# Performance work log

Measured on AMD Instinct MI355X. Metric: run time of the kernel, lower is better.

Reference implementation:

```python
import jax, jax.numpy as jnp
import numpy as np

N_ADDR, N_TX = 150000, 200000
IN_DIM, HID, HEADS = 64, 32, 4
DIM = HID // HEADS
E_AT, E_TA, E_AA = 1000000, 1000000, 500000
SLOPE = 0.2  # HANConv default negative_slope


def setup_inputs() -> dict:
    key = jax.random.key(0)
    ks = jax.random.split(key, 16)
    f = lambda k, shape, s: jax.random.normal(k, shape, dtype=jnp.float32) * s
    return {
        "x_addr": f(ks[0], (N_ADDR, IN_DIM), 1.0),
        "x_tx": f(ks[1], (N_TX, IN_DIM), 1.0),
        "e_at_src": jax.random.randint(ks[2], (E_AT,), 0, N_ADDR, dtype=jnp.int32),
        "e_at_dst": jax.random.randint(ks[3], (E_AT,), 0, N_TX, dtype=jnp.int32),
        "e_ta_src": jax.random.randint(ks[4], (E_TA,), 0, N_TX, dtype=jnp.int32),
        "e_ta_dst": jax.random.randint(ks[5], (E_TA,), 0, N_ADDR, dtype=jnp.int32),
        "e_aa_src": jax.random.randint(ks[6], (E_AA,), 0, N_ADDR, dtype=jnp.int32),
        "e_aa_dst": jax.random.randint(ks[7], (E_AA,), 0, N_ADDR, dtype=jnp.int32),
        "pW1": f(ks[8], (2, IN_DIM, HID), 0.1),      # layer-1 proj per node type [addr, tx]
        "pb1": jnp.zeros((2, HID), jnp.float32),
        "pW23": f(ks[9], (2, 2, HID, HID), 0.1),     # [layer-1, node_type]
        "pb23": jnp.zeros((2, 2, HID), jnp.float32),
        "att_src": f(ks[10], (3, 3, HEADS, DIM), 0.1),  # [layer, edge_type, H, D]
        "att_dst": f(ks[11], (3, 3, HEADS, DIM), 0.1),
        "kW": f(ks[12], (3, HID, HID), 0.1),         # semantic k_lin per layer
        "kb": jnp.zeros((3, HID), jnp.float32),
        "q": f(ks[13], (3, HID), 0.1),               # semantic query per layer
        "linW": f(ks[14], (HID, 2), 0.1),
        "linb": jnp.zeros((2,), jnp.float32),
    }


def _edge_softmax(logits, dst, n):
    # numerically stable segment softmax over destination neighborhoods
    m = jax.ops.segment_max(logits, dst, num_segments=n)          # [n, H]
    m = jnp.where(jnp.isfinite(m), m, 0.0)
    e = jnp.exp(logits - m[dst])
    s = jax.ops.segment_sum(e, dst, num_segments=n)
    return e / (s[dst] + 1e-16)


def _relation(h_src, h_dst, src, dst, a_s, a_d, n_dst):
    alpha_src = jnp.einsum('nhd,hd->nh', h_src, a_s)
    alpha_dst = jnp.einsum('nhd,hd->nh', h_dst, a_d)
    logit = alpha_src[src] + alpha_dst[dst]                        # [E, H]
    logit = jnp.where(logit >= 0, logit, SLOPE * logit)            # leaky_relu
    alpha = _edge_softmax(logit, dst, n_dst)
    msg = h_src[src] * alpha[:, :, None]                           # [E, H, D]
    out = jax.ops.segment_sum(msg, dst, num_segments=n_dst)        # [n_dst, H, D]
    return jax.nn.relu(out.reshape(n_dst, HID))


def _semantic(xs, kW, kb, q):
    # xs: [R, N, F]; semantic-level attention over R relations (PyG `group`)
    t = jnp.tanh(xs @ kW + kb).mean(axis=1)       # [R, F]
    attn = jax.nn.softmax((t * q).sum(-1))        # [R]
    return jnp.einsum('r,rnf->nf', attn, xs)


def _han_layer(x_a, x_t, Wa, ba, Wt, bt, a_s, a_d, kW, kb, q, edges):
    h_a = (x_a @ Wa + ba).reshape(-1, HEADS, DIM)
    h_t = (x_t @ Wt + bt).reshape(-1, HEADS, DIM)
    o_tx = _relation(h_a, h_t, edges[0], edges[1], a_s[0], a_d[0], N_TX)
    o_a1 = _relation(h_t, h_a, edges[2], edges[3], a_s[1], a_d[1], N_ADDR)
    o_a2 = _relation(h_a, h_a, edges[4], edges[5], a_s[2], a_d[2], N_ADDR)
    new_a = _semantic(jnp.stack([o_a1, o_a2]), kW, kb, q)
    new_t = _semantic(o_tx[None], kW, kb, q)
    return new_a, new_t


def reference(x_addr, x_tx, e_at_src, e_at_dst, e_ta_src, e_ta_dst,
              e_aa_src, e_aa_dst, pW1, pb1, pW23, pb23, att_src, att_dst,
              kW, kb, q, linW, linb):
    edges = (e_at_src, e_at_dst, e_ta_src, e_ta_dst, e_aa_src, e_aa_dst)
    a, t = _han_layer(x_addr, x_tx, pW1[0], pb1[0], pW1[1], pb1[1],
                      att_src[0], att_dst[0], kW[0], kb[0], q[0], edges)
    a, t = jax.nn.relu(a), jax.nn.relu(t)  # wrapper relu; dropout = eval identity
    for l in range(2):
        a, t = _han_layer(a, t, pW23[l, 0], pb23[l, 0], pW23[l, 1], pb23[l, 1],
                          att_src[l + 1], att_dst[l + 1],
                          kW[l + 1], kb[l + 1], q[l + 1], edges)
        a, t = jax.nn.relu(a), jax.nn.relu(t)
    return a @ linW + linb
```

## Files before the change

### kernel.cpp

```cpp
#include <hip/hip_runtime.h>
#include <hip/hip_bf16.h>
#include <hip/hip_fp16.h>

#define NA 150000
#define NT 200000
#define E_AT 1000000
#define E_TA 1000000
#define E_AA 500000

#define CHK 4096
#define CAP 8192
#define P_AT 391
#define P_TA 293
#define P_AA 293
#define NBINS (P_AT + P_TA + P_AA)
#define CB_AT 245
#define CB_TA 245
#define CB_AA 123
#define NBBIN (CB_AT + CB_TA + CB_AA)

#define GB_AT 6250
#define GB_TA 4688
#define GB_AA 4688

#define GA32 4688
#define GT32 6250
#define NB_SEM 586

#define WO_W1   0
#define WO_B1   4096
#define WO_W23  4160
#define WO_B23  8256
#define WO_AS   8384
#define WO_AD   8672
#define WO_KW   8960
#define WO_KB   12032
#define WO_Q    12128
#define WO_LW   12224
#define WO_LB   12288

__device__ __forceinline__ float ldf(const void* p, long i, int f32) {
    if (f32) return ((const float*)p)[i];
    unsigned int u = ((const unsigned short*)p)[i];
    union { unsigned int ui; float f; } v; v.ui = u << 16;
    return v.f;
}
__device__ __forceinline__ float bf2f(unsigned short u) {
    union { unsigned int ui; float f; } v; v.ui = ((unsigned int)u) << 16;
    return v.f;
}
__device__ __forceinline__ float h2f(unsigned short u) {
    return __half2float(__ushort_as_half(u));
}
__device__ __forceinline__ unsigned short f2h(float x) {
    return __half_as_ushort(__float2half(x));
}
__device__ __forceinline__ float ftanh(float x) {
    x = fminf(fmaxf(x, -9.f), 9.f);
    float e = __expf(2.f * x);
    return (e - 1.f) / (e + 1.f);
}

__global__ void k_init(const void* __restrict__ x,
                       const void* __restrict__ pW1, const void* __restrict__ pb1,
                       const void* __restrict__ pW23, const void* __restrict__ pb23,
                       const void* __restrict__ attS, const void* __restrict__ attD,
                       const void* __restrict__ kW, const void* __restrict__ kb,
                       const void* __restrict__ qv, const void* __restrict__ linW,
                       const void* __restrict__ linb,
                       float* __restrict__ wts, int* __restrict__ flagp,
                       int* __restrict__ gcnt, float* __restrict__ sem) {
    __shared__ int cnt;
    const int t = threadIdx.x;
    if (t == 0) cnt = 0;
    __syncthreads();
    const unsigned short* u = (const unsigned short*)x;
    int wild = 0;
    for (int i = t; i < 4096; i += 256) {
        unsigned short v = u[i];
        int e = (v >> 7) & 0xFF;
        if (e > 133 || (e != 0 && e < 100)) wild++;
        else if (e == 0 && (v & 0x7F)) wild++;
    }
    atomicAdd(&cnt, wild);
    __syncthreads();
    const int f32 = (cnt > 1024) ? 1 : 0;
    if (t == 0) *flagp = f32;
    if (t < 8) sem[t] = 0.f;
    for (int i = t; i < 1024; i += 256) gcnt[i] = 0;
    for (int i = t; i < 4096; i += 256) wts[WO_W1 + i]  = ldf(pW1, i, f32);
    for (int i = t; i < 64;   i += 256) wts[WO_B1 + i]  = ldf(pb1, i, f32);
    for (int i = t; i < 4096; i += 256) wts[WO_W23 + i] = ldf(pW23, i, f32);
    for (int i = t; i < 128;  i += 256) wts[WO_B23 + i] = ldf(pb23, i, f32);
    for (int i = t; i < 288;  i += 256) wts[WO_AS + i]  = ldf(attS, i, f32);
    for (int i = t; i < 288;  i += 256) wts[WO_AD + i]  = ldf(attD, i, f32);
    for (int i = t; i < 3072; i += 256) wts[WO_KW + i]  = ldf(kW, i, f32);
    for (int i = t; i < 96;   i += 256) wts[WO_KB + i]  = ldf(kb, i, f32);
    for (int i = t; i < 96;   i += 256) wts[WO_Q + i]   = ldf(qv, i, f32);
    for (int i = t; i < 64;   i += 256) wts[WO_LW + i]  = ldf(linW, i, f32);
    for (int i = t; i < 2;    i += 256) wts[WO_LB + i]  = ldf(linb, i, f32);
}

__global__ __launch_bounds__(256) void k_projbin(
        const void* __restrict__ Xa, const void* __restrict__ Xt,
        const float* __restrict__ W, const float* __restrict__ Bv,
        unsigned short* __restrict__ Ha, unsigned short* __restrict__ Ht,
        const float* __restrict__ attD,
        float* __restrict__ ad0, float* __restrict__ ad1, float* __restrict__ ad2,
        const int* __restrict__ flagp,
        const int* __restrict__ eat_s, const int* __restrict__ eat_d,
        const int* __restrict__ eta_s, const int* __restrict__ eta_d,
        const int* __restrict__ eaa_s, const int* __restrict__ eaa_d,
        int* __restrict__ gcnt,
        int* __restrict__ slot_at, int* __restrict__ slot_ta, int* __restrict__ slot_aa) {
    __shared__ float smem[4224];
    const int t = threadIdx.x;
    int b = blockIdx.x;
    if (b < NBBIN) {
        int* hist = (int*)smem;
        const int *src, *dst; int E, P, seg; int* slot;
        if (b < CB_AT)              { src = eat_s; dst = eat_d; E = E_AT; P = P_AT; seg = 0;            slot = slot_at; }
        else if (b < CB_AT + CB_TA) { b -= CB_AT;  src = eta_s; dst = eta_d; E = E_TA; P = P_TA; seg = P_AT;        slot = slot_ta; }
        else                        { b -= CB_AT + CB_TA; src = eaa_s; dst = eaa_d; E = E_AA; P = P_AA; seg = P_AT + P_TA; slot = slot_aa; }
        long e0 = (long)b * CHK;
        for (int i = t; i < P; i += 256) hist[i] = 0;
        __syncthreads();
        for (int k = 0; k < CHK; k += 256) {
            long e = e0 + k + t;
            if (e < E) atomicAdd(&hist[dst[e] >> 9], 1);
        }
        __syncthreads();
        for (int i = t; i < P; i += 256) {
            int v = hist[i];
            hist[i] = atomicAdd(&gcnt[seg + i], v);
        }
        __syncthreads();
        for (int k = 0; k < CHK; k += 256) {
            long e = e0 + k + t;
            if (e < E) {
                int d = dst[e];
                int bin = d >> 9;
                int pos = atomicAdd(&hist[bin], 1);
                slot[bin * CAP + pos] = ((d & 511) << 18) | src[e];
            }
        }
        return;
    }
    b -= NBBIN;
    constexpr int K = 64, XS = K + 4, CPR = K / 4, TOT4 = 32 * CPR;
    float* Xs = smem;
    float* Wl = smem + 2176;
    const bool isA = b < GA32;
    const int bb = isA ? b : b - GA32;
    const int N = isA ? NA : NT;
    const int wOff = isA ? 0 : 2048;
    const int bOff = isA ? 0 : 32;
    const long n0 = (long)bb * 32;
    for (int i = t; i < K * 32; i += 256) Wl[i] = W[wOff + i];
    {
        const void* X = isA ? Xa : Xt;
        const int f32 = *flagp;
        if (f32) {
            const float* Xf = (const float*)X;
            for (int i = t; i < TOT4; i += 256) {
                int r = i / CPR, c = (i - r * CPR) * 4;
                long gr = n0 + r; if (gr >= N) gr = N - 1;
                *(float4*)&Xs[r * XS + c] = *(const float4*)&Xf[gr * K + c];
            }
        } else {
            const unsigned short* Xh = (const unsigned short*)X;
            for (int i = t; i < TOT4; i += 256) {
                int r = i / CPR, c = (i - r * CPR) * 4;
                long gr = n0 + r; if (gr >= N) gr = N - 1;
                ushort4 v = *(const ushort4*)&Xh[gr * K + c];
                float4 o;
                o.x = bf2f(v.x); o.y = bf2f(v.y); o.z = bf2f(v.z); o.w = bf2f(v.w);
                *(float4*)&Xs[r * XS + c] = o;
            }
        }
    }
    __syncthreads();
    const int g = t >> 3, q = t & 7;
    const long n = n0 + g;
    float a0 = Bv[bOff + q * 4 + 0];
    float a1 = Bv[bOff + q * 4 + 1];
    float a2 = Bv[bOff + q * 4 + 2];
    float a3 = Bv[bOff + q * 4 + 3];
#pragma unroll 4
    for (int k4 = 0; k4 < K; k4 += 4) {
        float4 xv = *(const float4*)&Xs[g * XS + k4];
        float4 w0 = *(const float4*)&Wl[(k4 + 0) * 32 + q * 4];
        float4 w1 = *(const float4*)&Wl[(k4 + 1) * 32 + q * 4];
        float4 w2 = *(const float4*)&Wl[(k4 + 2) * 32 + q * 4];
        float4 w3 = *(const float4*)&Wl[(k4 + 3) * 32 + q * 4];
        a0 = fmaf(xv.x, w0.x, a0); a1 = fmaf(xv.x, w0.y, a1);
        a2 = fmaf(xv.x, w0.z, a2); a3 = fmaf(xv.x, w0.w, a3);
        a0 = fmaf(xv.y, w1.x, a0); a1 = fmaf(xv.y, w1.y, a1);
        a2 = fmaf(xv.y, w1.z, a2); a3 = fmaf(xv.y, w1.w, a3);
        a0 = fmaf(xv.z, w2.x, a0); a1 = fmaf(xv.z, w2.y, a1);
        a2 = fmaf(xv.z, w2.z, a2); a3 = fmaf(xv.z, w2.w, a3);
        a0 = fmaf(xv.w, w3.x, a0); a1 = fmaf(xv.w, w3.y, a1);
        a2 = fmaf(xv.w, w3.z, a2); a3 = fmaf(xv.w, w3.w, a3);
    }
    if (n < N) {
        unsigned short* Hh = isA ? Ha : Ht;
        unsigned int p01 = (unsigned)f2h(a0) | ((unsigned)f2h(a1) << 16);
        unsigned int p23 = (unsigned)f2h(a2) | ((unsigned)f2h(a3) << 16);
        *(uint2*)&Hh[n * 32 + q * 4] = make_uint2(p01, p23);
        const int hh = q >> 1;
        const int ai = q * 4;
        if (isA) {
            float p1 = a0 * attD[ai + 32] + a1 * attD[ai + 33]
                     + a2 * attD[ai + 34] + a3 * attD[ai + 35];
            float p2 = a0 * attD[ai + 64] + a1 * attD[ai + 65]
                     + a2 * attD[ai + 66] + a3 * attD[ai + 67];
            float s1 = p1 + __shfl_xor(p1, 1);
            float s2 = p2 + __shfl_xor(p2, 1);
            if (!(q & 1)) { ad1[n * 4 + hh] = s1; ad2[n * 4 + hh] = s2; }
        } else {
            float p0 = a0 * attD[ai] + a1 * attD[ai + 1]
                     + a2 * attD[ai + 2] + a3 * attD[ai + 3];
            float s0 = p0 + __shfl_xor(p0, 1);
            if (!(q & 1)) ad0[n * 4 + hh] = s0;
        }
    }
}

__global__ __launch_bounds__(256) void k_proj2(
        const float* __restrict__ O1, const float* __restrict__ Ot,
        const float* __restrict__ O2, const float* __restrict__ semL,
        const float* __restrict__ W, int wOffA, int wOffT,
        const float* __restrict__ Bv, int bOffA, int bOffT,
        unsigned short* __restrict__ Ha, unsigned short* __restrict__ Ht,
        const float* __restrict__ attD, int lBase,
        float* __restrict__ ad0, float* __restrict__ ad1, float* __restrict__ ad2) {
    constexpr int K = 32, XS = K + 4, CPR = K / 4, TOT4 = 32 * CPR;
    __shared__ float Xs[32 * XS];
    __shared__ float Wl[K * 32];
    const int t = threadIdx.x;
    const bool isA = blockIdx.x < GA32;
    const int bb = isA ? (int)blockIdx.x : (int)blockIdx.x - GA32;
    const int N = isA ? NA : NT;
    const int wOff = isA ? wOffA : wOffT;
    const int bOff = isA ? bOffA : bOffT;
    const long n0 = (long)bb * 32;
    for (int i = t; i < K * 32; i += 256) Wl[i] = W[wOff + i];
    if (isA) {
        float s0 = semL[0] * (1.0f / NA), s1 = semL[1] * (1.0f / NA);
        float m = fmaxf(s0, s1);
        float e0 = __expf(s0 - m), e1 = __expf(s1 - m);
        float inv = 1.f / (e0 + e1);
        const float w0 = e0 * inv, w1 = e1 * inv;
        for (int i = t; i < TOT4; i += 256) {
            int r = i / CPR, c = (i - r * CPR) * 4;
            long gr = n0 + r; if (gr >= N) gr = N - 1;
            float4 va = *(const float4*)&O1[gr * K + c];
            float4 vb = *(const float4*)&O2[gr * K + c];
            float4 o;
            o.x = fmaxf(w0 * va.x + w1 * vb.x, 0.f);
            o.y = fmaxf(w0 * va.y + w1 * vb.y, 0.f);
            o.z = fmaxf(w0 * va.z + w1 * vb.z, 0.f);
            o.w = fmaxf(w0 * va.w + w1 * vb.w, 0.f);
            *(float4*)&Xs[r * XS + c] = o;
        }
    } else {
        for (int i = t; i < TOT4; i += 256) {
            int r = i / CPR, c = (i - r * CPR) * 4;
            long gr = n0 + r; if (gr >= N) gr = N - 1;
            *(float4*)&Xs[r * XS + c] = *(const float4*)&Ot[gr * K + c];
        }
    }
    __syncthreads();
    const int g = t >> 3, q = t & 7;
    const long n = n0 + g;
    float a0 = Bv[bOff + q * 4 + 0];
    float a1 = Bv[bOff + q * 4 + 1];
    float a2 = Bv[bOff + q * 4 + 2];
    float a3 = Bv[bOff + q * 4 + 3];
#pragma unroll 4
    for (int k4 = 0; k4 < K; k4 += 4) {
        float4 xv = *(const float4*)&Xs[g * XS + k4];
        float4 w0 = *(const float4*)&Wl[(k4 + 0) * 32 + q * 4];
        float4 w1 = *(const float4*)&Wl[(k4 + 1) * 32 + q * 4];
        float4 w2 = *(const float4*)&Wl[(k4 + 2) * 32 + q * 4];
        float4 w3 = *(const float4*)&Wl[(k4 + 3) * 32 + q * 4];
        a0 = fmaf(xv.x, w0.x, a0); a1 = fmaf(xv.x, w0.y, a1);
        a2 = fmaf(xv.x, w0.z, a2); a3 = fmaf(xv.x, w0.w, a3);
        a0 = fmaf(xv.y, w1.x, a0); a1 = fmaf(xv.y, w1.y, a1);
        a2 = fmaf(xv.y, w1.z, a2); a3 = fmaf(xv.y, w1.w, a3);
        a0 = fmaf(xv.z, w2.x, a0); a1 = fmaf(xv.z, w2.y, a1);
        a2 = fmaf(xv.z, w2.z, a2); a3 = fmaf(xv.z, w2.w, a3);
        a0 = fmaf(xv.w, w3.x, a0); a1 = fmaf(xv.w, w3.y, a1);
        a2 = fmaf(xv.w, w3.z, a2); a3 = fmaf(xv.w, w3.w, a3);
    }
    if (n < N) {
        unsigned short* Hh = isA ? Ha : Ht;
        unsigned int p01 = (unsigned)f2h(a0) | ((unsigned)f2h(a1) << 16);
        unsigned int p23 = (unsigned)f2h(a2) | ((unsigned)f2h(a3) << 16);
        *(uint2*)&Hh[n * 32 + q * 4] = make_uint2(p01, p23);
        const int hh = q >> 1;
        const int ai = lBase + q * 4;
        if (isA) {
            float p1 = a0 * attD[ai + 32] + a1 * attD[ai + 33]
                     + a2 * attD[ai + 34] + a3 * attD[ai + 35];
            float p2 = a0 * attD[ai + 64] + a1 * attD[ai + 65]
                     + a2 * attD[ai + 66] + a3 * attD[ai + 67];
            float s1 = p1 + __shfl_xor(p1, 1);
            float s2 = p2 + __shfl_xor(p2, 1);
            if (!(q & 1)) { ad1[n * 4 + hh] = s1; ad2[n * 4 + hh] = s2; }
        } else {
            float p0 = a0 * attD[ai] + a1 * attD[ai + 1]
                     + a2 * attD[ai + 2] + a3 * attD[ai + 3];
            float s0 = p0 + __shfl_xor(p0, 1);
            if (!(q & 1)) ad0[n * 4 + hh] = s0;
        }
    }
}

__global__ __launch_bounds__(256) void k_binsort(
        const int* __restrict__ gcnt,
        const int* __restrict__ slot_at, const int* __restrict__ slot_ta,
        const int* __restrict__ slot_aa,
        int* __restrict__ off_at, int* __restrict__ off_ta, int* __restrict__ off_aa,
        int* __restrict__ csr_at, int* __restrict__ csr_ta, int* __restrict__ csr_aa) {
    __shared__ int sa[512], sb[512], cur[512];
    __shared__ int red[4];
    int b = blockIdx.x, t = threadIdx.x;
    const int* slot; int* off; int* csr; int N, bin, seg;
    if (b < P_AT)              { slot = slot_at; off = off_at; csr = csr_at; N = NT; bin = b;                seg = 0; }
    else if (b < P_AT + P_TA)  { slot = slot_ta; off = off_ta; csr = csr_ta; N = NA; bin = b - P_AT;         seg = P_AT; }
    else                       { slot = slot_aa; off = off_aa; csr = csr_aa; N = NA; bin = b - P_AT - P_TA;  seg = P_AT + P_TA; }
    if (b == 0 && t == 0) { off_at[NT] = E_AT; off_ta[NA] = E_TA; off_aa[NA] = E_AA; }
    int part = 0;
    for (int i = t; i < bin; i += 256) part += gcnt[seg + i];
    for (int o = 32; o > 0; o >>= 1) part += __shfl_xor(part, o, 64);
    if ((t & 63) == 0) red[t >> 6] = part;
    sa[t] = 0; sa[t + 256] = 0;
    __syncthreads();
    const int base = red[0] + red[1] + red[2] + red[3];
    const int cnt  = gcnt[seg + bin];
    const int* sp = &slot[bin * CAP];
    for (int i = t; i < cnt; i += 256) atomicAdd(&sa[sp[i] >> 18], 1);
    __syncthreads();
    int* in = sa; int* out = sb;
    for (int o = 1; o < 512; o <<= 1) {
        for (int i = t; i < 512; i += 256)
            out[i] = in[i] + (i >= o ? in[i - o] : 0);
        __syncthreads();
        int* tmp = in; in = out; out = tmp;
    }
    for (int i = t; i < 512; i += 256) {
        int excl = i ? in[i - 1] : 0;
        cur[i] = excl;
        int gd = bin * 512 + i;
        if (gd < N) off[gd] = base + excl;
    }
    __syncthreads();
    for (int i = t; i < cnt; i += 256) {
        int pk = sp[i];
        int pos = atomicAdd(&cur[pk >> 18], 1);
        csr[base + pos] = pk & 0x3FFFF;
    }
}

__global__ __launch_bounds__(256) void k_gather3(
        const int* __restrict__ off_at, const int* __restrict__ csr_at,
        const int* __restrict__ off_ta, const int* __restrict__ csr_ta,
        const int* __restrict__ off_aa, const int* __restrict__ csr_aa,
        const float* __restrict__ ad0, const float* __restrict__ ad1,
        const float* __restrict__ ad2,
        const unsigned short* __restrict__ h_a, const unsigned short* __restrict__ h_t,
        float* __restrict__ o_tx, float* __restrict__ o_a1, float* __restrict__ o_a2,
        const float* __restrict__ attS, int lBase, int gbAT) {
    int b = blockIdx.x;
    const int *off, *csr;
    const float *ad_;
    const unsigned short* Hs;
    float* O;
    int N, attOff;
    if (b < gbAT) {
        off = off_at; csr = csr_at; ad_ = ad0; Hs = h_a; O = o_tx; N = NT;
        attOff = lBase;
    } else if (b < gbAT + GB_TA) {
        b -= gbAT;
        off = off_ta; csr = csr_ta; ad_ = ad1; Hs = h_t; O = o_a1; N = NA;
        attOff = lBase + 32;
    } else {
        b -= gbAT + GB_TA;
        off = off_aa; csr = csr_aa; ad_ = ad2; Hs = h_a; O = o_a2; N = NA;
        attOff = lBase + 64;
    }
    const int t = threadIdx.x;
    const int q = t & 7;
    const int hh = q >> 1;
    const int n = b * 32 + (t >> 3);
    if (n >= N) return;
    const float4 aq = *(const float4*)&attS[attOff + q * 4];
    const float aq0 = aq.x, aq1 = aq.y, aq2 = aq.z, aq3 = aq.w;
    const float adv = ad_[n * 4 + hh];
    const int p0 = off[n], p1 = off[n + 1];
    float ax = 0.f, ay = 0.f, az = 0.f, aw = 0.f, se = 0.f;
    int p = p0;
    for (; p + 4 <= p1; p += 4) {
        int s0 = csr[p], s1 = csr[p + 1], s2 = csr[p + 2], s3 = csr[p + 3];
        ushort4 v0 = *(const ushort4*)&Hs[s0 * 32 + q * 4];
        ushort4 v1 = *(const ushort4*)&Hs[s1 * 32 + q * 4];
        ushort4 v2 = *(const ushort4*)&Hs[s2 * 32 + q * 4];
        ushort4 v3 = *(const ushort4*)&Hs[s3 * 32 + q * 4];
        float h00 = h2f(v0.x), h01 = h2f(v0.y), h02 = h2f(v0.z), h03 = h2f(v0.w);
        float h10 = h2f(v1.x), h11 = h2f(v1.y), h12 = h2f(v1.z), h13 = h2f(v1.w);
        float h20 = h2f(v2.x), h21 = h2f(v2.y), h22 = h2f(v2.z), h23 = h2f(v2.w);
        float h30 = h2f(v3.x), h31 = h2f(v3.y), h32 = h2f(v3.z), h33 = h2f(v3.w);
        float pt0 = h00 * aq0 + h01 * aq1 + h02 * aq2 + h03 * aq3;
        float pt1 = h10 * aq0 + h11 * aq1 + h12 * aq2 + h13 * aq3;
        float pt2 = h20 * aq0 + h21 * aq1 + h22 * aq2 + h23 * aq3;
        float pt3 = h30 * aq0 + h31 * aq1 + h32 * aq2 + h33 * aq3;
        float al0 = pt0 + __shfl_xor(pt0, 1);
        float al1 = pt1 + __shfl_xor(pt1, 1);
        float al2 = pt2 + __shfl_xor(pt2, 1);
        float al3 = pt3 + __shfl_xor(pt3, 1);
        float l0 = al0 + adv; l0 = fmaxf(l0, 0.2f * l0); float e0 = __expf(l0);
        float l1 = al1 + adv; l1 = fmaxf(l1, 0.2f * l1); float e1 = __expf(l1);
        float l2 = al2 + adv; l2 = fmaxf(l2, 0.2f * l2); float e2 = __expf(l2);
        float l3 = al3 + adv; l3 = fmaxf(l3, 0.2f * l3); float e3 = __expf(l3);
        se += e0 + e1 + e2 + e3;
        ax += e0 * h00 + e1 * h10 + e2 * h20 + e3 * h30;
        ay += e0 * h01 + e1 * h11 + e2 * h21 + e3 * h31;
        az += e0 * h02 + e1 * h12 + e2 * h22 + e3 * h32;
        aw += e0 * h03 + e1 * h13 + e2 * h23 + e3 * h33;
    }
    for (; p < p1; p++) {
        int s = csr[p];
        ushort4 v = *(const ushort4*)&Hs[s * 32 + q * 4];
        float h0 = h2f(v.x), h1 = h2f(v.y), h2 = h2f(v.z), h3 = h2f(v.w);
        float pt = h0 * aq0 + h1 * aq1 + h2 * aq2 + h3 * aq3;
        float al = pt + __shfl_xor(pt, 1);
        float l = al + adv; l = fmaxf(l, 0.2f * l);
        float e = __expf(l);
        se += e;
        ax += e * h0; ay += e * h1; az += e * h2; aw += e * h3;
    }
    const float inv = 1.f / (se + 1e-16f);
    float4 r;
    r.x = fmaxf(ax * inv, 0.f);
// ... 32 lines not shown
        }
    }
    for (int o = 32; o > 0; o >>= 1) S += __shfl_xor(S, o, 64);
    if ((t & 63) == 0) atomicAdd(&bacc, S);
    __syncthreads();
    if (t == 0) atomicAdd(&semL[r], bacc);
}

__global__ void k_combine_final(const float* __restrict__ o1, const float* __restrict__ o2,
                                const float* __restrict__ semL,
                                const float* __restrict__ linW, const float* __restrict__ linb,
                                void* __restrict__ out, int N, const int* __restrict__ flagp) {
    int n = blockIdx.x * blockDim.x + threadIdx.x;
    if (n >= N) return;
    int f32 = *flagp;
    float q0 = semL[0] * (1.0f / NA), q1 = semL[1] * (1.0f / NA);
    float m = fmaxf(q0, q1);
    float e0 = __expf(q0 - m), e1 = __expf(q1 - m);
    float ai = 1.f / (e0 + e1);
    float w0 = e0 * ai, w1 = e1 * ai;
    float s0 = linb[0], s1 = linb[1];
    const float* p1 = &o1[(long)n * 32];
    const float* p2 = &o2[(long)n * 32];
#pragma unroll
    for (int f = 0; f < 32; f++) {
        float v = w0 * p1[f] + w1 * p2[f];
        v = (v > 0.f) ? v : 0.f;
        s0 += v * linW[f * 2];
        s1 += v * linW[f * 2 + 1];
    }
    if (f32) { ((float*)out)[n * 2] = s0; ((float*)out)[n * 2 + 1] = s1; }
    else {
        ((__hip_bfloat16*)out)[n * 2] = __float2bfloat16(s0);
        ((__hip_bfloat16*)out)[n * 2 + 1] = __float2bfloat16(s1);
    }
}

static inline int gblocks(long n) { return (int)((n + 255) / 256); }

extern "C" void kernel_launch(void* const* d_in, const int* in_sizes, int n_in,
                              void* d_out, int out_size, void* d_ws, size_t ws_size,
                              hipStream_t stream) {
    const void* x_addr = d_in[0];
    const void* x_tx   = d_in[1];
    const int* eat_s = (const int*)d_in[2];
    const int* eat_d = (const int*)d_in[3];
    const int* eta_s = (const int*)d_in[4];
    const int* eta_d = (const int*)d_in[5];
    const int* eaa_s = (const int*)d_in[6];
    const int* eaa_d = (const int*)d_in[7];
    const void* pW1  = d_in[8];
    const void* pb1  = d_in[9];
    const void* pW23 = d_in[10];
    const void* pb23 = d_in[11];
    const void* attS = d_in[12];
    const void* attD = d_in[13];
    const void* kW   = d_in[14];
    const void* kb   = d_in[15];
    const void* qv   = d_in[16];
    const void* linW = d_in[17];
    const void* linb = d_in[18];

    const size_t NA32 = (size_t)NA * 32, NT32 = (size_t)NT * 32;
    const size_t NA4 = (size_t)NA * 4, NT4 = (size_t)NT * 4;

    float* ws    = (float*)d_ws;
    float* h_aF  = ws;
    float* h_tF  = h_aF + NA32;
    float* o_a1  = h_tF + NT32;
    float* o_a2  = o_a1 + NA32;
    float* o_tx  = o_a2 + NA32;
    float* ad1   = o_tx + NT32;
    float* ad2   = ad1 + NA4;
    float* ad0   = ad2 + NA4;
    float* sem   = ad0 + NT4;
    int*   flagp = (int*)(sem + 8);
    int*   off_at = flagp + 16;
    int*   off_ta = off_at + (NT + 1);
    int*   off_aa = off_ta + (NA + 1);
    int*   csr_at = off_aa + (NA + 1);
    int*   csr_ta = csr_at + E_AT;
    int*   csr_aa = csr_ta + E_TA;
    int*   gcnt   = csr_aa + E_AA;
    int*   slot_at = gcnt + 1024;
    int*   slot_ta = slot_at + P_AT * CAP;
    int*   slot_aa = slot_ta + P_TA * CAP;
    float* wts    = (float*)(slot_aa + (size_t)P_AA * CAP);

    unsigned short* h_a = (unsigned short*)h_aF;
    unsigned short* h_t = (unsigned short*)h_tF;

    k_init<<<1, 256, 0, stream>>>(x_addr, pW1, pb1, pW23, pb23, attS, attD,
                                  kW, kb, qv, linW, linb, wts, flagp, gcnt, sem);

    k_projbin<<<NBBIN + GA32 + GT32, 256, 0, stream>>>(
        x_addr, x_tx, wts + WO_W1, wts + WO_B1, h_a, h_t, wts + WO_AD,
        ad0, ad1, ad2, flagp,
        eat_s, eat_d, eta_s, eta_d, eaa_s, eaa_d,
        gcnt, slot_at, slot_ta, slot_aa);
    k_binsort<<<NBINS, 256, 0, stream>>>(gcnt, slot_at, slot_ta, slot_aa,
                                         off_at, off_ta, off_aa, csr_at, csr_ta, csr_aa);

    for (int l = 0; l < 3; l++) {
        if (l > 0) {
            int wi = (l - 1) * 2;
            k_proj2<<<GA32 + GT32, 256, 0, stream>>>(
                o_a1, o_tx, o_a2, sem + 2 * (l - 1),
                wts + WO_W23, (wi + 0) * 1024, (wi + 1) * 1024,
                wts + WO_B23, (wi + 0) * 32, (wi + 1) * 32,
                h_a, h_t, wts + WO_AD, l * 96, ad0, ad1, ad2);
        }
        const int gbAT = (l < 2) ? GB_AT : 0;
        k_gather3<<<gbAT + GB_TA + GB_AA, 256, 0, stream>>>(
            off_at, csr_at, off_ta, csr_ta, off_aa, csr_aa,
            ad0, ad1, ad2, h_a, h_t, o_tx, o_a1, o_a2, wts + WO_AS, l * 96, gbAT);
        k_sem_reduce<<<2 * NB_SEM, 256, 0, stream>>>(
            o_a1, o_a2, wts + WO_KW + l * 1024, wts + WO_KB + l * 32,
            wts + WO_Q + l * 32, sem + 2 * l);
        if (l == 2) {
            k_combine_final<<<gblocks(NA), 256, 0, stream>>>(o_a1, o_a2, sem + 4,
                                                             wts + WO_LW, wts + WO_LB,
                                                             d_out, NA, flagp);
        }
    }
}
```

Measured before the change: 547.1 us.

## Replace bin-sort CSR build with degree count, scan, and atomic scatter

CSR construction no longer goes through bucketed slot buffers and a per-bin local sort. The new path does a global per-node degree count with atomics (fused with weight init), a per-bin offset scan, and then scatters each source index straight into its CSR position using a global atomic cursor. The goal is to drop the large intermediate slot array and its second pass. Neighbour order within each row now depends on atomic scheduling, and the scatter issues many more global atomics. Separately, the projection kernels now compute 64 rows per block instead of 32, with two accumulator sets per thread, to improve reuse of the weights held in shared memory.

```diff
diff --git a/kernel.cpp b/kernel.cpp
--- a/kernel.cpp
+++ b/kernel.cpp
@@ -9,7 +9,6 @@
 #define E_AA 500000
 
 #define CHK 4096
-#define CAP 8192
 #define P_AT 391
 #define P_TA 293
 #define P_AA 293
@@ -23,8 +22,8 @@
 #define GB_TA 4688
 #define GB_AA 4688
 
-#define GA32 4688
-#define GT32 6250
+#define GA64 2344
+#define GT64 3125
 #define NB_SEM 586
 
 #define WO_W1   0
@@ -61,47 +60,110 @@
     return (e - 1.f) / (e + 1.f);
 }
 
-__global__ void k_init(const void* __restrict__ x,
-                       const void* __restrict__ pW1, const void* __restrict__ pb1,
-                       const void* __restrict__ pW23, const void* __restrict__ pb23,
-                       const void* __restrict__ attS, const void* __restrict__ attD,
-                       const void* __restrict__ kW, const void* __restrict__ kb,
-                       const void* __restrict__ qv, const void* __restrict__ linW,
-                       const void* __restrict__ linb,
-                       float* __restrict__ wts, int* __restrict__ flagp,
-                       int* __restrict__ gcnt, float* __restrict__ sem) {
-    __shared__ int cnt;
+__global__ __launch_bounds__(256) void k_countinit(
+        const int* __restrict__ eat_d, const int* __restrict__ eta_d,
+        const int* __restrict__ eaa_d,
+        int* __restrict__ gcnt, int* __restrict__ deg_at,
+        int* __restrict__ deg_ta, int* __restrict__ deg_aa,
+        const void* __restrict__ x,
+        const void* __restrict__ pW1, const void* __restrict__ pb1,
+        const void* __restrict__ pW23, const void* __restrict__ pb23,
+        const void* __restrict__ attS, const void* __restrict__ attD,
+        const void* __restrict__ kW, const void* __restrict__ kb,
+        const void* __restrict__ qv, const void* __restrict__ linW,
+        const void* __restrict__ linb,
+        float* __restrict__ wts, int* __restrict__ flagp, float* __restrict__ sem) {
+    __shared__ int hist[P_AT];
     const int t = threadIdx.x;
-    if (t == 0) cnt = 0;
+    int b = blockIdx.x;
+    if (b >= NBBIN) {
+        if (t == 0) hist[0] = 0;
+        __syncthreads();
+        const unsigned short* u = (const unsigned short*)x;
+        int wild = 0;
+        for (int i = t; i < 4096; i += 256) {
+            unsigned short v = u[i];
+            int e = (v >> 7) & 0xFF;
+            if (e > 133 || (e != 0 && e < 100)) wild++;
+            else if (e == 0 && (v & 0x7F)) wild++;
+        }
+        atomicAdd(&hist[0], wild);
+        __syncthreads();
+        const int f32 = (hist[0] > 1024) ? 1 : 0;
+        if (t == 0) *flagp = f32;
+        if (t < 8) sem[t] = 0.f;
+        for (int i = t; i < 4096; i += 256) wts[WO_W1 + i]  = ldf(pW1, i, f32);
+        for (int i = t; i < 64;   i += 256) wts[WO_B1 + i]  = ldf(pb1, i, f32);
+        for (int i = t; i < 4096; i += 256) wts[WO_W23 + i] = ldf(pW23, i, f32);
+        for (int i = t; i < 128;  i += 256) wts[WO_B23 + i] = ldf(pb23, i, f32);
+        for (int i = t; i < 288;  i += 256) wts[WO_AS + i]  = ldf(attS, i, f32);
+        for (int i = t; i < 288;  i += 256) wts[WO_AD + i]  = ldf(attD, i, f32);
+        for (int i = t; i < 3072; i += 256) wts[WO_KW + i]  = ldf(kW, i, f32);
+        for (int i = t; i < 96;   i += 256) wts[WO_KB + i]  = ldf(kb, i, f32);
+        for (int i = t; i < 96;   i += 256) wts[WO_Q + i]   = ldf(qv, i, f32);
+        for (int i = t; i < 64;   i += 256) wts[WO_LW + i]  = ldf(linW, i, f32);
+        for (int i = t; i < 2;    i += 256) wts[WO_LB + i]  = ldf(linb, i, f32);
+        return;
+    }
+    const int* dst; int E, P, seg; int* deg;
+    if (b < CB_AT)              { dst = eat_d; E = E_AT; P = P_AT; seg = 0;            deg = deg_at; }
+    else if (b < CB_AT + CB_TA) { b -= CB_AT;  dst = eta_d; E = E_TA; P = P_TA; seg = P_AT;        deg = deg_ta; }
+    else                        { b -= CB_AT + CB_TA; dst = eaa_d; E = E_AA; P = P_AA; seg = P_AT + P_TA; deg = deg_aa; }
+    long e0 = (long)b * CHK;
+    for (int i = t; i < P; i += 256) hist[i] = 0;
     __syncthreads();
-    const unsigned short* u = (const unsigned short*)x;
-    int wild = 0;
-    for (int i = t; i < 4096; i += 256) {
-        unsigned short v = u[i];
-        int e = (v >> 7) & 0xFF;
-        if (e > 133 || (e != 0 && e < 100)) wild++;
-        else if (e == 0 && (v & 0x7F)) wild++;
-    }
-    atomicAdd(&cnt, wild);
+    for (int k = 0; k < CHK; k += 256) {
+        long e = e0 + k + t;
+        if (e < E) {
+            int d = dst[e];
+            atomicAdd(&deg[d], 1);
+            atomicAdd(&hist[d >> 9], 1);
+        }
+    }
     __syncthreads();
-    const int f32 = (cnt > 1024) ? 1 : 0;
-    if (t == 0) *flagp = f32;
-    if (t < 8) sem[t] = 0.f;
-    for (int i = t; i < 1024; i += 256) gcnt[i] = 0;
-    for (int i = t; i < 4096; i += 256) wts[WO_W1 + i]  = ldf(pW1, i, f32);
-    for (int i = t; i < 64;   i += 256) wts[WO_B1 + i]  = ldf(pb1, i, f32);
-    for (int i = t; i < 4096; i += 256) wts[WO_W23 + i] = ldf(pW23, i, f32);
-    for (int i = t; i < 128;  i += 256) wts[WO_B23 + i] = ldf(pb23, i, f32);
-    for (int i = t; i < 288;  i += 256) wts[WO_AS + i]  = ldf(attS, i, f32);
-    for (int i = t; i < 288;  i += 256) wts[WO_AD + i]  = ldf(attD, i, f32);
-    for (int i = t; i < 3072; i += 256) wts[WO_KW + i]  = ldf(kW, i, f32);
-    for (int i = t; i < 96;   i += 256) wts[WO_KB + i]  = ldf(kb, i, f32);
-    for (int i = t; i < 96;   i += 256) wts[WO_Q + i]   = ldf(qv, i, f32);
-    for (int i = t; i < 64;   i += 256) wts[WO_LW + i]  = ldf(linW, i, f32);
-    for (int i = t; i < 2;    i += 256) wts[WO_LB + i]  = ldf(linb, i, f32);
-}
-
-__global__ __launch_bounds__(256) void k_projbin(
+    for (int i = t; i < P; i += 256)
+        if (hist[i]) atomicAdd(&gcnt[seg + i], hist[i]);
+}
+
+__global__ __launch_bounds__(256) void k_offscan(
+        const int* __restrict__ gcnt,
+        const int* __restrict__ deg_at, const int* __restrict__ deg_ta,
+        const int* __restrict__ deg_aa,
+        int* __restrict__ off_at, int* __restrict__ off_ta, int* __restrict__ off_aa,
+        int* __restrict__ cur_at, int* __restrict__ cur_ta, int* __restrict__ cur_aa) {
+    __shared__ int sa[512], sb[512];
+    __shared__ int red[4];
+    int b = blockIdx.x, t = threadIdx.x;
+    const int* deg; int* off; int* cur; int N, bin, seg;
+    if (b < P_AT)              { deg = deg_at; off = off_at; cur = cur_at; N = NT; bin = b;                seg = 0; }
+    else if (b < P_AT + P_TA)  { deg = deg_ta; off = off_ta; cur = cur_ta; N = NA; bin = b - P_AT;         seg = P_AT; }
+    else                       { deg = deg_aa; off = off_aa; cur = cur_aa; N = NA; bin = b - P_AT - P_TA;  seg = P_AT + P_TA; }
+    if (b == 0 && t == 0) { off_at[NT] = E_AT; off_ta[NA] = E_TA; off_aa[NA] = E_AA; }
+    int part = 0;
+    for (int i = t; i < bin; i += 256) part += gcnt[seg + i];
+    for (int o = 32; o > 0; o >>= 1) part += __shfl_xor(part, o, 64);
+    if ((t & 63) == 0) red[t >> 6] = part;
+    for (int i = t; i < 512; i += 256) {
+        int gd = bin * 512 + i;
+        sa[i] = (gd < N) ? deg[gd] : 0;
+    }
+    __syncthreads();
+    const int base = red[0] + red[1] + red[2] + red[3];
+    int* in = sa; int* out = sb;
+    for (int o = 1; o < 512; o <<= 1) {
+        for (int i = t; i < 512; i += 256)
+            out[i] = in[i] + (i >= o ? in[i - o] : 0);
+        __syncthreads();
+        int* tmp = in; in = out; out = tmp;
+    }
+    for (int i = t; i < 512; i += 256) {
+        int excl = i ? in[i - 1] : 0;
+        int gd = bin * 512 + i;
+        if (gd < N) { off[gd] = base + excl; cur[gd] = base + excl; }
+    }
+}
+
+__global__ __launch_bounds__(256) void k_projscat(
         const void* __restrict__ Xa, const void* __restrict__ Xt,
         const float* __restrict__ W, const float* __restrict__ Bv,
         unsigned short* __restrict__ Ha, unsigned short* __restrict__ Ht,
@@ -111,51 +173,37 @@
         const int* __restrict__ eat_s, const int* __restrict__ eat_d,
         const int* __restrict__ eta_s, const int* __restrict__ eta_d,
         const int* __restrict__ eaa_s, const int* __restrict__ eaa_d,
-        int* __restrict__ gcnt,
-        int* __restrict__ slot_at, int* __restrict__ slot_ta, int* __restrict__ slot_aa) {
-    __shared__ float smem[4224];
+        int* __restrict__ cur_at, int* __restrict__ cur_ta, int* __restrict__ cur_aa,
+        int* __restrict__ csr_at, int* __restrict__ csr_ta, int* __restrict__ csr_aa) {
+    __shared__ float smem[6400];
     const int t = threadIdx.x;
     int b = blockIdx.x;
     if (b < NBBIN) {
-        int* hist = (int*)smem;
-        const int *src, *dst; int E, P, seg; int* slot;
-        if (b < CB_AT)              { src = eat_s; dst = eat_d; E = E_AT; P = P_AT; seg = 0;            slot = slot_at; }
-        else if (b < CB_AT + CB_TA) { b -= CB_AT;  src = eta_s; dst = eta_d; E = E_TA; P = P_TA; seg = P_AT;        slot = slot_ta; }
-        else                        { b -= CB_AT + CB_TA; src = eaa_s; dst = eaa_d; E = E_AA; P = P_AA; seg = P_AT + P_TA; slot = slot_aa; }
+        const int *src, *dst; int E; int* cur; int* csr;
+        if (b < CB_AT)              { src = eat_s; dst = eat_d; E = E_AT; cur = cur_at; csr = csr_at; }
+        else if (b < CB_AT + CB_TA) { b -= CB_AT;  src = eta_s; dst = eta_d; E = E_TA; cur = cur_ta; csr = csr_ta; }
+        else                        { b -= CB_AT + CB_TA; src = eaa_s; dst = eaa_d; E = E_AA; cur = cur_aa; csr = csr_aa; }
         long e0 = (long)b * CHK;
-        for (int i = t; i < P; i += 256) hist[i] = 0;
-        __syncthreads();
-        for (int k = 0; k < CHK; k += 256) {
-            long e = e0 + k + t;
-            if (e < E) atomicAdd(&hist[dst[e] >> 9], 1);
-        }
-        __syncthreads();
-        for (int i = t; i < P; i += 256) {
-            int v = hist[i];
-            hist[i] = atomicAdd(&gcnt[seg + i], v);
-        }
-        __syncthreads();
         for (int k = 0; k < CHK; k += 256) {
             long e = e0 + k + t;
             if (e < E) {
                 int d = dst[e];
-                int bin = d >> 9;
-                int pos = atomicAdd(&hist[bin], 1);
-                slot[bin * CAP + pos] = ((d & 511) << 18) | src[e];
+                int pos = atomicAdd(&cur[d], 1);
+                csr[pos] = src[e];
             }
         }
         return;
     }
     b -= NBBIN;
-    constexpr int K = 64, XS = K + 4, CPR = K / 4, TOT4 = 32 * CPR;
+    constexpr int K = 64, XS = K + 4, CPR = K / 4, TOT4 = 64 * CPR;
     float* Xs = smem;
-    float* Wl = smem + 2176;
-    const bool isA = b < GA32;
-    const int bb = isA ? b : b - GA32;
+    float* Wl = smem + 4352;
+    const bool isA = b < GA64;
+    const int bb = isA ? b : b - GA64;
     const int N = isA ? NA : NT;
     const int wOff = isA ? 0 : 2048;
     const int bOff = isA ? 0 : 32;
-    const long n0 = (long)bb * 32;
+    const long n0 = (long)bb * 64;
     for (int i = t; i < K * 32; i += 256) Wl[i] = W[wOff + i];
     {
         const void* X = isA ? Xa : Xt;
@@ -163,14 +211,14 @@
         if (f32) {
             const float* Xf = (const float*)X;
             for (int i = t; i < TOT4; i += 256) {
-                int r = i / CPR, c = (i - r * CPR) * 4;
+                int r = i / CPR, c = (i & (CPR - 1)) * 4;
                 long gr = n0 + r; if (gr >= N) gr = N - 1;
                 *(float4*)&Xs[r * XS + c] = *(const float4*)&Xf[gr * K + c];
             }
         } else {
             const unsigned short* Xh = (const unsigned short*)X;
             for (int i = t; i < TOT4; i += 256) {
-                int r = i / CPR, c = (i - r * CPR) * 4;
+                int r = i / CPR, c = (i & (CPR - 1)) * 4;
                 long gr = n0 + r; if (gr >= N) gr = N - 1;
                 ushort4 v = *(const ushort4*)&Xh[gr * K + c];
                 float4 o;
@@ -181,47 +229,74 @@
     }
     __syncthreads();
     const int g = t >> 3, q = t & 7;
-    const long n = n0 + g;
-    float a0 = Bv[bOff + q * 4 + 0];
-    float a1 = Bv[bOff + q * 4 + 1];
-    float a2 = Bv[bOff + q * 4 + 2];
-    float a3 = Bv[bOff + q * 4 + 3];
-#pragma unroll 4
+    const long nA = n0 + g, nB = n0 + g + 32;
+    float A0 = Bv[bOff + q * 4 + 0], A1 = Bv[bOff + q * 4 + 1];
+    float A2 = Bv[bOff + q * 4 + 2], A3 = Bv[bOff + q * 4 + 3];
+    float B0 = A0, B1 = A1, B2 = A2, B3 = A3;
+#pragma unroll 2
     for (int k4 = 0; k4 < K; k4 += 4) {
-        float4 xv = *(const float4*)&Xs[g * XS + k4];
+        float4 xa = *(const float4*)&Xs[g * XS + k4];
+        float4 xb = *(const float4*)&Xs[(g + 32) * XS + k4];
         float4 w0 = *(const float4*)&Wl[(k4 + 0) * 32 + q * 4];
         float4 w1 = *(const float4*)&Wl[(k4 + 1) * 32 + q * 4];
         float4 w2 = *(const float4*)&Wl[(k4 + 2) * 32 + q * 4];
         float4 w3 = *(const float4*)&Wl[(k4 + 3) * 32 + q * 4];
-        a0 = fmaf(xv.x, w0.x, a0); a1 = fmaf(xv.x, w0.y, a1);
-        a2 = fmaf(xv.x, w0.z, a2); a3 = fmaf(xv.x, w0.w, a3);
-        a0 = fmaf(xv.y, w1.x, a0); a1 = fmaf(xv.y, w1.y, a1);
-        a2 = fmaf(xv.y, w1.z, a2); a3 = fmaf(xv.y, w1.w, a3);
-        a0 = fmaf(xv.z, w2.x, a0); a1 = fmaf(xv.z, w2.y, a1);
-        a2 = fmaf(xv.z, w2.z, a2); a3 = fmaf(xv.z, w2.w, a3);
-        a0 = fmaf(xv.w, w3.x, a0); a1 = fmaf(xv.w, w3.y, a1);
-        a2 = fmaf(xv.w, w3.z, a2); a3 = fmaf(xv.w, w3.w, a3);
-    }
-    if (n < N) {
-        unsigned short* Hh = isA ? Ha : Ht;
-        unsigned int p01 = (unsigned)f2h(a0) | ((unsigned)f2h(a1) << 16);
-        unsigned int p23 = (unsigned)f2h(a2) | ((unsigned)f2h(a3) << 16);
-        *(uint2*)&Hh[n * 32 + q * 4] = make_uint2(p01, p23);
-        const int hh = q >> 1;
-        const int ai = q * 4;
+        A0 = fmaf(xa.x, w0.x, A0); A1 = fmaf(xa.x, w0.y, A1);
+        A2 = fmaf(xa.x, w0.z, A2); A3 = fmaf(xa.x, w0.w, A3);
+        B0 = fmaf(xb.x, w0.x, B0); B1 = fmaf(xb.x, w0.y, B1);
+        B2 = fmaf(xb.x, w0.z, B2); B3 = fmaf(xb.x, w0.w, B3);
+        A0 = fmaf(xa.y, w1.x, A0); A1 = fmaf(xa.y, w1.y, A1);
+        A2 = fmaf(xa.y, w1.z, A2); A3 = fmaf(xa.y, w1.w, A3);
+        B0 = fmaf(xb.y, w1.x, B0); B1 = fmaf(xb.y, w1.y, B1);
+        B2 = fmaf(xb.y, w1.z, B2); B3 = fmaf(xb.y, w1.w, B3);
+        A0 = fmaf(xa.z, w2.x, A0); A1 = fmaf(xa.z, w2.y, A1);
+        A2 = fmaf(xa.z, w2.z, A2); A3 = fmaf(xa.z, w2.w, A3);
+        B0 = fmaf(xb.z, w2.x, B0); B1 = fmaf(xb.z, w2.y, B1);
+        B2 = fmaf(xb.z, w2.z, B2); B3 = fmaf(xb.z, w2.w, B3);
+        A0 = fmaf(xa.w, w3.x, A0); A1 = fmaf(xa.w, w3.y, A1);
+        A2 = fmaf(xa.w, w3.z, A2); A3 = fmaf(xa.w, w3.w, A3);
+        B0 = fmaf(xb.w, w3.x, B0); B1 = fmaf(xb.w, w3.y, B1);
+        B2 = fmaf(xb.w, w3.z, B2); B3 = fmaf(xb.w, w3.w, B3);
+    }
+    const int hh = q >> 1;
+    const int ai = q * 4;
+    unsigned short* Hh = isA ? Ha : Ht;
+    if (nA < N) {
+        unsigned int p01 = (unsigned)f2h(A0) | ((unsigned)f2h(A1) << 16);
+        unsigned int p23 = (unsigned)f2h(A2) | ((unsigned)f2h(A3) << 16);
+        *(uint2*)&Hh[nA * 32 + q * 4] = make_uint2(p01, p23);
         if (isA) {
-            float p1 = a0 * attD[ai + 32] + a1 * attD[ai + 33]
-                     + a2 * attD[ai + 34] + a3 * attD[ai + 35];
-            float p2 = a0 * attD[ai + 64] + a1 * attD[ai + 65]
-                     + a2 * attD[ai + 66] + a3 * attD[ai + 67];
+            float p1 = A0 * attD[ai + 32] + A1 * attD[ai + 33]
+                     + A2 * attD[ai + 34] + A3 * attD[ai + 35];
+            float p2 = A0 * attD[ai + 64] + A1 * attD[ai + 65]
+                     + A2 * attD[ai + 66] + A3 * attD[ai + 67];
             float s1 = p1 + __shfl_xor(p1, 1);
             float s2 = p2 + __shfl_xor(p2, 1);
-            if (!(q & 1)) { ad1[n * 4 + hh] = s1; ad2[n * 4 + hh] = s2; }
+            if (!(q & 1)) { ad1[nA * 4 + hh] = s1; ad2[nA * 4 + hh] = s2; }
         } else {
-            float p0 = a0 * attD[ai] + a1 * attD[ai + 1]
-                     + a2 * attD[ai + 2] + a3 * attD[ai + 3];
+            float p0 = A0 * attD[ai] + A1 * attD[ai + 1]
+                     + A2 * attD[ai + 2] + A3 * attD[ai + 3];
             float s0 = p0 + __shfl_xor(p0, 1);
-            if (!(q & 1)) ad0[n * 4 + hh] = s0;
+            if (!(q & 1)) ad0[nA * 4 + hh] = s0;
+        }
+    }
+    if (nB < N) {
+        unsigned int p01 = (unsigned)f2h(B0) | ((unsigned)f2h(B1) << 16);
+        unsigned int p23 = (unsigned)f2h(B2) | ((unsigned)f2h(B3) << 16);
+        *(uint2*)&Hh[nB * 32 + q * 4] = make_uint2(p01, p23);
+        if (isA) {
+            float p1 = B0 * attD[ai + 32] + B1 * attD[ai + 33]
+                     + B2 * attD[ai + 34] + B3 * attD[ai + 35];
+            float p2 = B0 * attD[ai + 64] + B1 * attD[ai + 65]
+                     + B2 * attD[ai + 66] + B3 * attD[ai + 67];
+            float s1 = p1 + __shfl_xor(p1, 1);
+            float s2 = p2 + __shfl_xor(p2, 1);
+            if (!(q & 1)) { ad1[nB * 4 + hh] = s1; ad2[nB * 4 + hh] = s2; }
+        } else {
+            float p0 = B0 * attD[ai] + B1 * attD[ai + 1]
+                     + B2 * attD[ai + 2] + B3 * attD[ai + 3];
+            float s0 = p0 + __shfl_xor(p0, 1);
+            if (!(q & 1)) ad0[nB * 4 + hh] = s0;
         }
     }
 }
@@ -234,16 +309,16 @@
         unsigned short* __restrict__ Ha, unsigned short* __restrict__ Ht,
         const float* __restrict__ attD, int lBase,
         float* __restrict__ ad0, float* __restrict__ ad1, float* __restrict__ ad2) {
-    constexpr int K = 32, XS = K + 4, CPR = K / 4, TOT4 = 32 * CPR;
-    __shared__ float Xs[32 * XS];
+    constexpr int K = 32, XS = K + 4, CPR = K / 4, TOT4 = 64 * CPR;
+    __shared__ float Xs[64 * XS];
     __shared__ float Wl[K * 32];
     const int t = threadIdx.x;
-    const bool isA = blockIdx.x < GA32;
-    const int bb = isA ? (int)blockIdx.x : (int)blockIdx.x - GA32;
+    const bool isA = blockIdx.x < GA64;
+    const int bb = isA ? (int)blockIdx.x : (int)blockIdx.x - GA64;
     const int N = isA ? NA : NT;
     const int wOff = isA ? wOffA : wOffT;
     const int bOff = isA ? bOffA : bOffT;
-    const long n0 = (long)bb * 32;
+    const long n0 = (long)bb * 64;
     for (int i = t; i < K * 32; i += 256) Wl[i] = W[wOff + i];
     if (isA) {
         float s0 = semL[0] * (1.0f / NA), s1 = semL[1] * (1.0f / NA);
@@ -252,7 +327,7 @@
         float inv = 1.f / (e0 + e1);
         const float w0 = e0 * inv, w1 = e1 * inv;
         for (int i = t; i < TOT4; i += 256) {
-            int r = i / CPR, c = (i - r * CPR) * 4;
+            int r = i / CPR, c = (i & (CPR - 1)) * 4;
             long gr = n0 + r; if (gr >= N) gr = N - 1;
             float4 va = *(const float4*)&O1[gr * K + c];
             float4 vb = *(const float4*)&O2[gr * K + c];
@@ -265,101 +340,82 @@
         }
     } else {
         for (int i = t; i < TOT4; i += 256) {
-            int r = i / CPR, c = (i - r * CPR) * 4;
+            int r = i / CPR, c = (i & (CPR - 1)) * 4;
             long gr = n0 + r; if (gr >= N) gr = N - 1;
             *(float4*)&Xs[r * XS + c] = *(const float4*)&Ot[gr * K + c];
         }
     }
     __syncthreads();
     const int g = t >> 3, q = t & 7;
-    const long n = n0 + g;
-    float a0 = Bv[bOff + q * 4 + 0];
-    float a1 = Bv[bOff + q * 4 + 1];
-    float a2 = Bv[bOff + q * 4 + 2];
-    float a3 = Bv[bOff + q * 4 + 3];
-#pragma unroll 4
+    const long nA = n0 + g, nB = n0 + g + 32;
+    float A0 = Bv[bOff + q * 4 + 0], A1 = Bv[bOff + q * 4 + 1];
+    float A2 = Bv[bOff + q * 4 + 2], A3 = Bv[bOff + q * 4 + 3];
+    float B0 = A0, B1 = A1, B2 = A2, B3 = A3;
+#pragma unroll 2
     for (int k4 = 0; k4 < K; k4 += 4) {
-        float4 xv = *(const float4*)&Xs[g * XS + k4];
+        float4 xa = *(const float4*)&Xs[g * XS + k4];
+        float4 xb = *(const float4*)&Xs[(g + 32) * XS + k4];
         float4 w0 = *(const float4*)&Wl[(k4 + 0) * 32 + q * 4];
         float4 w1 = *(const float4*)&Wl[(k4 + 1) * 32 + q * 4];
         float4 w2 = *(const float4*)&Wl[(k4 + 2) * 32 + q * 4];
         float4 w3 = *(const float4*)&Wl[(k4 + 3) * 32 + q * 4];
-        a0 = fmaf(xv.x, w0.x, a0); a1 = fmaf(xv.x, w0.y, a1);
-        a2 = fmaf(xv.x, w0.z, a2); a3 = fmaf(xv.x, w0.w, a3);
-        a0 = fmaf(xv.y, w1.x, a0); a1 = fmaf(xv.y, w1.y, a1);
-        a2 = fmaf(xv.y, w1.z, a2); a3 = fmaf(xv.y, w1.w, a3);
-        a0 = fmaf(xv.z, w2.x, a0); a1 = fmaf(xv.z, w2.y, a1);
-        a2 = fmaf(xv.z, w2.z, a2); a3 = fmaf(xv.z, w2.w, a3);
-        a0 = fmaf(xv.w, w3.x, a0); a1 = fmaf(xv.w, w3.y, a1);
-        a2 = fmaf(xv.w, w3.z, a2); a3 = fmaf(xv.w, w3.w, a3);
-    }
-    if (n < N) {
-        unsigned short* Hh = isA ? Ha : Ht;
-        unsigned int p01 = (unsigned)f2h(a0) | ((unsigned)f2h(a1) << 16);
-        unsigned int p23 = (unsigned)f2h(a2) | ((unsigned)f2h(a3) << 16);
-        *(uint2*)&Hh[n * 32 + q * 4] = make_uint2(p01, p23);
-        const int hh = q >> 1;
-        const int ai = lBase + q * 4;
+        A0 = fmaf(xa.x, w0.x, A0); A1 = fmaf(xa.x, w0.y, A1);
+        A2 = fmaf(xa.x, w0.z, A2); A3 = fmaf(xa.x, w0.w, A3);
+        B0 = fmaf(xb.x, w0.x, B0); B1 = fmaf(xb.x, w0.y, B1);
+        B2 = fmaf(xb.x, w0.z, B2); B3 = fmaf(xb.x, w0.w, B3);
+        A0 = fmaf(xa.y, w1.x, A0); A1 = fmaf(xa.y, w1.y, A1);
+        A2 = fmaf(xa.y, w1.z, A2); A3 = fmaf(xa.y, w1.w, A3);
+        B0 = fmaf(xb.y, w1.x, B0); B1 = fmaf(xb.y, w1.y, B1);
+        B2 = fmaf(xb.y, w1.z, B2); B3 = fmaf(xb.y, w1.w, B3);
+        A0 = fmaf(xa.z, w2.x, A0); A1 = fmaf(xa.z, w2.y, A1);
+        A2 = fmaf(xa.z, w2.z, A2); A3 = fmaf(xa.z, w2.w, A3);
+        B0 = fmaf(xb.z, w2.x, B0); B1 = fmaf(xb.z, w2.y, B1);
+        B2 = fmaf(xb.z, w2.z, B2); B3 = fmaf(xb.z, w2.w, B3);
+        A0 = fmaf(xa.w, w3.x, A0); A1 = fmaf(xa.w, w3.y, A1);
+        A2 = fmaf(xa.w, w3.z, A2); A3 = fmaf(xa.w, w3.w, A3);
+        B0 = fmaf(xb.w, w3.x, B0); B1 = fmaf(xb.w, w3.y, B1);
+        B2 = fmaf(xb.w, w3.z, B2); B3 = fmaf(xb.w, w3.w, B3);
+    }
+    const int hh = q >> 1;
+    const int ai = lBase + q * 4;
+    unsigned short* Hh = isA ? Ha : Ht;
+    if (nA < N) {
+        unsigned int p01 = (unsigned)f2h(A0) | ((unsigned)f2h(A1) << 16);
+        unsigned int p23 = (unsigned)f2h(A2) | ((unsigned)f2h(A3) << 16);
+        *(uint2*)&Hh[nA * 32 + q * 4] = make_uint2(p01, p23);
         if (isA) {
-            float p1 = a0 * attD[ai + 32] + a1 * attD[ai + 33]
-                     + a2 * attD[ai + 34] + a3 * attD[ai + 35];
-            float p2 = a0 * attD[ai + 64] + a1 * attD[ai + 65]
-                     + a2 * attD[ai + 66] + a3 * attD[ai + 67];
+            float p1 = A0 * attD[ai + 32] + A1 * attD[ai + 33]
+                     + A2 * attD[ai + 34] + A3 * attD[ai + 35];
+            float p2 = A0 * attD[ai + 64] + A1 * attD[ai + 65]
+                     + A2 * attD[ai + 66] + A3 * attD[ai + 67];
             float s1 = p1 + __shfl_xor(p1, 1);
             float s2 = p2 + __shfl_xor(p2, 1);
-            if (!(q & 1)) { ad1[n * 4 + hh] = s1; ad2[n * 4 + hh] = s2; }
+            if (!(q & 1)) { ad1[nA * 4 + hh] = s1; ad2[nA * 4 + hh] = s2; }
         } else {
-            float p0 = a0 * attD[ai] + a1 * attD[ai + 1]
-                     + a2 * attD[ai + 2] + a3 * attD[ai + 3];
+            float p0 = A0 * attD[ai] + A1 * attD[ai + 1]
+                     + A2 * attD[ai + 2] + A3 * attD[ai + 3];
             float s0 = p0 + __shfl_xor(p0, 1);
-            if (!(q & 1)) ad0[n * 4 + hh] = s0;
-        }
-    }
-}
-
-__global__ __launch_bounds__(256) void k_binsort(
-        const int* __restrict__ gcnt,
-        const int* __restrict__ slot_at, const int* __restrict__ slot_ta,
-        const int* __restrict__ slot_aa,
-        int* __restrict__ off_at, int* __restrict__ off_ta, int* __restrict__ off_aa,
-        int* __restrict__ csr_at, int* __restrict__ csr_ta, int* __restrict__ csr_aa) {
-    __shared__ int sa[512], sb[512], cur[512];
-    __shared__ int red[4];
-    int b = blockIdx.x, t = threadIdx.x;
-    const int* slot; int* off; int* csr; int N, bin, seg;
-    if (b < P_AT)              { slot = slot_at; off = off_at; csr = csr_at; N = NT; bin = b;                seg = 0; }
-    else if (b < P_AT + P_TA)  { slot = slot_ta; off = off_ta; csr = csr_ta; N = NA; bin = b - P_AT;         seg = P_AT; }
-    else                       { slot = slot_aa; off = off_aa; csr = csr_aa; N = NA; bin = b - P_AT - P_TA;  seg = P_AT + P_TA; }
-    if (b == 0 && t == 0) { off_at[NT] = E_AT; off_ta[NA] = E_TA; off_aa[NA] = E_AA; }
-    int part = 0;
-    for (int i = t; i < bin; i += 256) part += gcnt[seg + i];
-    for (int o = 32; o > 0; o >>= 1) part += __shfl_xor(part, o, 64);
-    if ((t & 63) == 0) red[t >> 6] = part;
-    sa[t] = 0; sa[t + 256] = 0;
-    __syncthreads();
-    const int base = red[0] + red[1] + red[2] + red[3];
-    const int cnt  = gcnt[seg + bin];
-    const int* sp = &slot[bin * CAP];
-    for (int i = t; i < cnt; i += 256) atomicAdd(&sa[sp[i] >> 18], 1);
-    __syncthreads();
-    int* in = sa; int* out = sb;
-    for (int o = 1; o < 512; o <<= 1) {
-        for (int i = t; i < 512; i += 256)
-            out[i] = in[i] + (i >= o ? in[i - o] : 0);
-        __syncthreads();
-        int* tmp = in; in = out; out = tmp;
-    }
-    for (int i = t; i < 512; i += 256) {
-        int excl = i ? in[i - 1] : 0;
-        cur[i] = excl;
-        int gd = bin * 512 + i;
-        if (gd < N) off[gd] = base + excl;
-    }
-    __syncthreads();
-    for (int i = t; i < cnt; i += 256) {
-        int pk = sp[i];
-        int pos = atomicAdd(&cur[pk >> 18], 1);
-        csr[base + pos] = pk & 0x3FFFF;
+            if (!(q & 1)) ad0[nA * 4 + hh] = s0;
+        }
+    }
+    if (nB < N) {
+        unsigned int p01 = (unsigned)f2h(B0) | ((unsigned)f2h(B1) << 16);
+        unsigned int p23 = (unsigned)f2h(B2) | ((unsigned)f2h(B3) << 16);
+        *(uint2*)&Hh[nB * 32 + q * 4] = make_uint2(p01, p23);
+        if (isA) {
+            float p1 = B0 * attD[ai + 32] + B1 * attD[ai + 33]
+                     + B2 * attD[ai + 34] + B3 * attD[ai + 35];
+            float p2 = B0 * attD[ai + 64] + B1 * attD[ai + 65]
+                     + B2 * attD[ai + 66] + B3 * attD[ai + 67];
+            float s1 = p1 + __shfl_xor(p1, 1);
+            float s2 = p2 + __shfl_xor(p2, 1);
+            if (!(q & 1)) { ad1[nB * 4 + hh] = s1; ad2[nB * 4 + hh] = s2; }
+        } else {
+            float p0 = B0 * attD[ai] + B1 * attD[ai + 1]
+                     + B2 * attD[ai + 2] + B3 * attD[ai + 3];
+            float s0 = p0 + __shfl_xor(p0, 1);
+            if (!(q & 1)) ad0[nB * 4 + hh] = s0;
+        }
     }
 }
 
@@ -558,29 +614,38 @@
     int*   csr_ta = csr_at + E_AT;
     int*   csr_aa = csr_ta + E_TA;
     int*   gcnt   = csr_aa + E_AA;
-    int*   slot_at = gcnt + 1024;
-    int*   slot_ta = slot_at + P_AT * CAP;
-    int*   slot_aa = slot_ta + P_TA * CAP;
-    float* wts    = (float*)(slot_aa + (size_t)P_AA * CAP);
+    int*   deg_at = gcnt + 1024;
+    int*   deg_ta = deg_at + NT;
+    int*   deg_aa = deg_ta + NA;
+    int*   cur_at = deg_aa + NA;
+    int*   cur_ta = cur_at + NT;
+    int*   cur_aa = cur_ta + NA;
+    float* wts    = (float*)(cur_aa + NA);
 
     unsigned short* h_a = (unsigned short*)h_aF;
     unsigned short* h_t = (unsigned short*)h_tF;
 
-    k_init<<<1, 256, 0, stream>>>(x_addr, pW1, pb1, pW23, pb23, attS, attD,
-                                  kW, kb, qv, linW, linb, wts, flagp, gcnt, sem);
-
-    k_projbin<<<NBBIN + GA32 + GT32, 256, 0, stream>>>(
+    (void)hipMemsetAsync(gcnt, 0, (size_t)(1024 + NT + 2 * NA) * sizeof(int), stream);
+
+    k_countinit<<<NBBIN + 1, 256, 0, stream>>>(
+        eat_d, eta_d, eaa_d, gcnt, deg_at, deg_ta, deg_aa,
+        x_addr, pW1, pb1, pW23, pb23, attS, attD, kW, kb, qv, linW, linb,
+        wts, flagp, sem);
+
+    k_offscan<<<NBINS, 256, 0, stream>>>(gcnt, deg_at, deg_ta, deg_aa,
+                                         off_at, off_ta, off_aa,
+                                         cur_at, cur_ta, cur_aa);
+
+    k_projscat<<<NBBIN + GA64 + GT64, 256, 0, stream>>>(
         x_addr, x_tx, wts + WO_W1, wts + WO_B1, h_a, h_t, wts + WO_AD,
         ad0, ad1, ad2, flagp,
         eat_s, eat_d, eta_s, eta_d, eaa_s, eaa_d,
-        gcnt, slot_at, slot_ta, slot_aa);
-    k_binsort<<<NBINS, 256, 0, stream>>>(gcnt, slot_at, slot_ta, slot_aa,
-                                         off_at, off_ta, off_aa, csr_at, csr_ta, csr_aa);
+        cur_at, cur_ta, cur_aa, csr_at, csr_ta, csr_aa);
 
     for (int l = 0; l < 3; l++) {
         if (l > 0) {
             int wi = (l - 1) * 2;
-            k_proj2<<<GA32 + GT32, 256, 0, stream>>>(
+            k_proj2<<<GA64 + GT64, 256, 0, stream>>>(
                 o_a1, o_tx, o_a2, sem + 2 * (l - 1),
                 wts + WO_W23, (wi + 0) * 1024, (wi + 1) * 1024,
                 wts + WO_B23, (wi + 0) * 32, (wi + 1) * 32,
```

After: 676.1 us. 1.24x slower.
